# Performance work log

Hardware: AMD Instinct MI355X
Metric: run time of the kernel (lower is better)

The kernel has to match this reference:

```python
import jax, jax.numpy as jnp
import numpy as np

B, V, F = 128, 256, 64      # batch, vertices, features-per-vertex
NS, NLR, K, NOUT = 4, 64, 40, 128
F_EFF = 2 * F               # cat_means doubles feature dim


def setup_inputs() -> dict:
    key = jax.random.key(0)
    k0, k1, k2 = jax.random.split(key, 3)
    x = jax.random.normal(k0, (B, V, F), dtype=jnp.float32)
    # f_slr: single Linear(F_EFF, NS+NLR) + ReLU (f_slr_depth=1)
    W_slr = jax.random.normal(k1, (F_EFF, NS + NLR), dtype=jnp.float32) / np.sqrt(F_EFF).astype(np.float32)
    b_slr = jnp.zeros((NS + NLR,), dtype=jnp.float32)
    # f_out: single Linear(F_EFF + 2*NLR, NOUT) + ReLU (f_out_depth=1, 2 agg methods)
    fin = F_EFF + 2 * NLR
    W_out = jax.random.normal(k2, (fin, NOUT), dtype=jnp.float32) / np.sqrt(fin).astype(np.float32)
    b_out = jnp.zeros((NOUT,), dtype=jnp.float32)
    return {"x": x, "W_slr": W_slr, "b_slr": b_slr, "W_out": W_out, "b_out": b_out}


def reference(x, W_slr, b_slr, W_out, b_out):
    # cat_means: append per-event feature means (broadcast over vertices)
    x = jnp.concatenate([x, jnp.broadcast_to(x.mean(axis=1, keepdims=True), x.shape)], axis=-1)  # (B,V,2F)
    slr = jax.nn.relu(x @ W_slr + b_slr)                    # (B,V,NS+NLR)
    s, lr = slr[..., :NS], slr[..., NS:]
    # pairwise squared distances in latent space (potential only needs d^2, so
    # we skip the sqrt: exp(-10*d^2) == exp(-10*d2), and kNN order is identical)
    diff = s[:, :, None, :] - s[:, None, :, :]              # (B,V,V,NS)
    d2 = jnp.sum(diff * diff, axis=-1)                      # (B,V,V)
    _, idx = jax.lax.top_k(-d2, K)                          # (B,V,K) k smallest (incl. self)
    d2k = jnp.take_along_axis(d2, idx, axis=2)              # (B,V,K)
    lr_nb = jax.vmap(lambda l, i: l[i])(lr, idx)            # (B,V,K,NLR)
    v = jnp.exp(-10.0 * d2k)                                # potential exp(-10 d^2)
    ft = lr_nb * v[..., None]                               # (B,V,K,NLR)
    fp = jnp.concatenate([x, ft.mean(axis=2), ft.max(axis=2)], axis=-1)  # (B,V,2F+2NLR)
    return jax.nn.relu(fp @ W_out + b_out)                  # (B,V,NOUT)
```

## Files before the change

kernel.cpp:

```cpp
#include <hip/hip_runtime.h>

constexpr int Bn = 128, Vn = 256, Fn = 64;
constexpr int NSLR = 68, NSn = 4, NLRn = 64;
constexpr int Kn = 40, NOUTn = 128;
constexpr int ROWS = Bn * Vn;
constexpr int KB2 = 192;

typedef __attribute__((ext_vector_type(8))) short short8;
typedef __attribute__((ext_vector_type(4))) float f32x4;

__device__ __forceinline__ int mbcnt64(unsigned long long m) {
  return __builtin_amdgcn_mbcnt_hi((unsigned)(m >> 32),
         __builtin_amdgcn_mbcnt_lo((unsigned)(m & 0xFFFFFFFFull), 0));
}
__device__ __forceinline__ unsigned short rneb(float v) {
  unsigned u = __float_as_uint(v);
  unsigned r = u + 0x7FFFu + ((u >> 16) & 1u);
  return (unsigned short)(r >> 16);
}
__device__ __forceinline__ float bf2f(unsigned short h) {
  return __uint_as_float(((unsigned)h) << 16);
}
#define GL_LDS(gp, lp) __builtin_amdgcn_global_load_lds( \
    (const __attribute__((address_space(1))) void*)(gp), \
    (__attribute__((address_space(3))) void*)(lp), 16, 0, 0)

__global__ __launch_bounds__(256) void kprep_w(const float* __restrict__ W_slr,
                                               const float* __restrict__ W_out,
                                               short* __restrict__ wt1h, short* __restrict__ wt1l,
                                               short* __restrict__ wt2) {
  const int col = blockIdx.x;
  const int t = threadIdx.x;
  if (t < 64) {
    float val = (col < NSLR) ? W_slr[t * NSLR + col] : 0.f;
    unsigned short h = rneb(val);
    wt1h[col * 64 + t] = (short)h;
    wt1l[col * 64 + t] = (short)rneb(val - bf2f(h));
  } else {
    int k = t - 64;
    int row = (k < 64) ? k : 64 + k;
    wt2[col * KB2 + k] = (short)rneb(W_out[row * NOUTn + col]);
  }
}

__global__ __launch_bounds__(256) void kprep_x(const float* __restrict__ x,
                                               short* __restrict__ xhi, short* __restrict__ xlo,
                                               float* __restrict__ xmean) {
  const int b = blockIdx.x, t = threadIdx.x;
  const int f4 = t & 15, vg = t >> 4;
  const float4* xb = (const float4*)(x + (size_t)b * 16384);
  float4 sum = make_float4(0.f, 0.f, 0.f, 0.f);
  for (int i = 0; i < 16; ++i) {
    int v = vg * 16 + i;
    float4 val = xb[v * 16 + f4];
    sum.x += val.x; sum.y += val.y; sum.z += val.z; sum.w += val.w;
    unsigned short h0 = rneb(val.x), h1 = rneb(val.y), h2 = rneb(val.z), h3 = rneb(val.w);
    short4 hi = {(short)h0, (short)h1, (short)h2, (short)h3};
    short4 lo = {(short)rneb(val.x - bf2f(h0)), (short)rneb(val.y - bf2f(h1)),
                 (short)rneb(val.z - bf2f(h2)), (short)rneb(val.w - bf2f(h3))};
    size_t o = (size_t)b * 4096 + v * 16 + f4;
    ((short4*)xhi)[o] = hi;
    ((short4*)xlo)[o] = lo;
  }
  __shared__ float4 ps[16][16];
  ps[vg][f4] = sum;
  __syncthreads();
  if (t < 16) {
    float4 m = ps[0][t];
    for (int g = 1; g < 16; ++g) {
      float4 v = ps[g][t];
      m.x += v.x; m.y += v.y; m.z += v.z; m.w += v.w;
    }
    m.x *= (1.f / 256.f); m.y *= (1.f / 256.f); m.z *= (1.f / 256.f); m.w *= (1.f / 256.f);
    ((float4*)xmean)[b * 16 + t] = m;
  }
}

__global__ __launch_bounds__(256) void kbias(const float* __restrict__ xmean,
                                             const float* __restrict__ W_slr,
                                             const float* __restrict__ b_slr,
                                             const float* __restrict__ W_out,
                                             const float* __restrict__ b_out,
                                             float* __restrict__ bias1,
                                             float* __restrict__ bias2) {
  const int b = blockIdx.x, t = threadIdx.x;
  __shared__ float xm[64];
  if (t < 64) xm[t] = xmean[b * 64 + t];
  __syncthreads();
  if (t < 128) {
    float acc = b_out[t];
    for (int f = 0; f < 64; ++f) acc = fmaf(xm[f], W_out[(64 + f) * NOUTn + t], acc);
    bias2[b * 128 + t] = acc;
  } else {
    int c = t - 128;
    float acc = 0.f;
    if (c < NSLR) {
      acc = b_slr[c];
      for (int f = 0; f < 64; ++f) acc = fmaf(xm[f], W_slr[(64 + f) * NSLR + c], acc);
    }
    bias1[b * 128 + c] = acc;
  }
}

__global__ __launch_bounds__(256) void kgemm1(
    const short* __restrict__ xhi, const short* __restrict__ xlo,
    const short* __restrict__ wt1h, const short* __restrict__ wt1l,
    const float* __restrict__ bias1,
    float* __restrict__ s_ws, float* __restrict__ lr_ws) {
  __shared__ __align__(16) short Ah[4096], Al[4096], Bh[8192], Bl[8192];
  const int t = threadIdx.x, l = t & 63, w = t >> 6;
  const int wr = w >> 1, wc = w & 1;
  const int rowBase = blockIdx.x * 64;
  const int b = rowBase >> 8;
  const int lr8 = l >> 3, ul = (l & 7) ^ lr8;

#pragma unroll
  for (int rep = 0; rep < 2; ++rep) {
    const int seg = w + rep * 4;
    size_t o = (size_t)(rowBase + seg * 8 + lr8) * 64 + ul * 8;
    GL_LDS(xhi + o, &Ah[seg * 512]);
    GL_LDS(xlo + o, &Al[seg * 512]);
  }
#pragma unroll
  for (int rep = 0; rep < 4; ++rep) {
    const int seg = w + rep * 4;
    size_t o = (size_t)(seg * 8 + lr8) * 64 + ul * 8;
    GL_LDS(wt1h + o, &Bh[seg * 512]);
    GL_LDS(wt1l + o, &Bl[seg * 512]);
  }
  __syncthreads();

  f32x4 acc[2][4];
#pragma unroll
  for (int mf = 0; mf < 2; ++mf)
#pragma unroll
    for (int nf = 0; nf < 4; ++nf) acc[mf][nf] = (f32x4)(0.f);

#pragma unroll
  for (int ks = 0; ks < 2; ++ks) {
    short8 ah[2], al[2], bh[4], bl[4];
#pragma unroll
    for (int mf = 0; mf < 2; ++mf) {
      int row = wr * 32 + mf * 16 + (l & 15);
      int pu = (ks * 4 + (l >> 4)) ^ (row & 7);
      ah[mf] = *(const short8*)&Ah[row * 64 + pu * 8];
      al[mf] = *(const short8*)&Al[row * 64 + pu * 8];
    }
#pragma unroll
    for (int nf = 0; nf < 4; ++nf) {
      int col = wc * 64 + nf * 16 + (l & 15);
      int pu = (ks * 4 + (l >> 4)) ^ (col & 7);
      bh[nf] = *(const short8*)&Bh[col * 64 + pu * 8];
      bl[nf] = *(const short8*)&Bl[col * 64 + pu * 8];
    }
#pragma unroll
    for (int mf = 0; mf < 2; ++mf)
#pragma unroll
      for (int nf = 0; nf < 4; ++nf) {
        acc[mf][nf] = __builtin_amdgcn_mfma_f32_16x16x32_bf16(ah[mf], bh[nf], acc[mf][nf], 0, 0, 0);
        acc[mf][nf] = __builtin_amdgcn_mfma_f32_16x16x32_bf16(ah[mf], bl[nf], acc[mf][nf], 0, 0, 0);
        acc[mf][nf] = __builtin_amdgcn_mfma_f32_16x16x32_bf16(al[mf], bh[nf], acc[mf][nf], 0, 0, 0);
      }
  }
#pragma unroll
  for (int mf = 0; mf < 2; ++mf)
#pragma unroll
    for (int nf = 0; nf < 4; ++nf) {
      const int col = wc * 64 + nf * 16 + (l & 15);
      if (col < NSLR) {
        const float bia = bias1[b * 128 + col];
#pragma unroll
        for (int r = 0; r < 4; ++r) {
          int row = rowBase + wr * 32 + mf * 16 + (l >> 4) * 4 + r;
          float vv = acc[mf][nf][r] + bia;
          vv = vv > 0.f ? vv : 0.f;
          if (col < NSn) s_ws[b * 1024 + col * 256 + (row & 255)] = vv;
          else           lr_ws[(size_t)row * NLRn + (col - NSn)] = vv;
        }
      }
    }
}

__global__ __launch_bounds__(256) void kgemm2(
    const short* __restrict__ xhi, const short* __restrict__ fm,
    const short* __restrict__ fx, const short* __restrict__ wt2,
    const float* __restrict__ bias2, float* __restrict__ outp) {
  __shared__ __align__(16) short As[4096], Bs[8192];
  const int t = threadIdx.x, l = t & 63, w = t >> 6;
  const int wr = w >> 1, wc = w & 1;
  const int rowBase = blockIdx.x * 64;
  const int b = rowBase >> 8;
  const int lr8 = l >> 3, ul = (l & 7) ^ lr8;

  f32x4 acc[2][4];
#pragma unroll
  for (int mf = 0; mf < 2; ++mf)
#pragma unroll
    for (int nf = 0; nf < 4; ++nf) acc[mf][nf] = (f32x4)(0.f);

#pragma unroll
  for (int kc = 0; kc < 3; ++kc) {
    __syncthreads();
    const short* asrc = (kc == 0) ? xhi : (kc == 1) ? fm : fx;
#pragma unroll
    for (int rep = 0; rep < 2; ++rep) {
      const int seg = w + rep * 4;
      size_t o = (size_t)(rowBase + seg * 8 + lr8) * 64 + ul * 8;
      GL_LDS(asrc + o, &As[seg * 512]);
    }
#pragma unroll
    for (int rep = 0; rep < 4; ++rep) {
      const int seg = w + rep * 4;
      size_t o = (size_t)(seg * 8 + lr8) * KB2 + kc * 64 + ul * 8;
      GL_LDS(wt2 + o, &Bs[seg * 512]);
    }
    __syncthreads();
#pragma unroll
    for (int ks = 0; ks < 2; ++ks) {
      short8 a[2], bb[4];
#pragma unroll
      for (int mf = 0; mf < 2; ++mf) {
        int row = wr * 32 + mf * 16 + (l & 15);
        int pu = (ks * 4 + (l >> 4)) ^ (row & 7);
        a[mf] = *(const short8*)&As[row * 64 + pu * 8];
      }
#pragma unroll
      for (int nf = 0; nf < 4; ++nf) {
        int col = wc * 64 + nf * 16 + (l & 15);
        int pu = (ks * 4 + (l >> 4)) ^ (col & 7);
        bb[nf] = *(const short8*)&Bs[col * 64 + pu * 8];
      }
#pragma unroll
      for (int mf = 0; mf < 2; ++mf)
#pragma unroll
        for (int nf = 0; nf < 4; ++nf)
          acc[mf][nf] = __builtin_amdgcn_mfma_f32_16x16x32_bf16(a[mf], bb[nf], acc[mf][nf], 0, 0, 0);
    }
  }
#pragma unroll
  for (int mf = 0; mf < 2; ++mf)
#pragma unroll
    for (int nf = 0; nf < 4; ++nf) {
      const int col = wc * 64 + nf * 16 + (l & 15);
      const float bia = bias2[b * 128 + col];
#pragma unroll
      for (int r = 0; r < 4; ++r) {
        int row = rowBase + wr * 32 + mf * 16 + (l >> 4) * 4 + r;
        float vv = acc[mf][nf][r] + bia;
        outp[(size_t)row * NOUTn + col] = vv > 0.f ? vv : 0.f;
      }
    }
}

__global__ __launch_bounds__(256) void kselect(const float* __restrict__ s_ws,
                                               const float* __restrict__ lr_ws,
                                               short* __restrict__ fm,
                                               short* __restrict__ fx) {
  __shared__ float sT[4][256];
  __shared__ unsigned int lst[4][Kn];
  const int id = blockIdx.x;
  const int xcd = id & 7;
  const int rrx = id >> 3;
  const int b = xcd + 8 * (rrx & 15);
  const int seg = rrx >> 4;
  const int t = threadIdx.x, lane = t & 63, w = t >> 6;

  {
    const float* sb = s_ws + b * 1024;
    sT[0][t] = sb[t]; sT[1][t] = sb[256 + t];
    sT[2][t] = sb[512 + t]; sT[3][t] = sb[768 + t];
  }
  __syncthreads();

  const float C = -14.4269504088896340736f;
  const float* lrbase = lr_ws + (size_t)b * (256 * NLRn) + lane;

  for (int it = 0; it < 4; ++it) {
    const int i = seg * 16 + w * 4 + it;
    const float si0 = sT[0][i], si1 = sT[1][i];
    const float si2 = sT[2][i], si3 = sT[3][i];
    unsigned int kb[4];
    float vv[4];
#pragma unroll
    for (int q = 0; q < 4; ++q) {
      int j = q * 64 + lane;
      float d0 = sT[0][j] - si0;
      float d1 = sT[1][j] - si1;
      float d2_ = sT[2][j] - si2;
      float d3 = sT[3][j] - si3;
      float dd = ((d0 * d0 + d1 * d1) + d2_ * d2_) + d3 * d3;
      kb[q] = __float_as_uint(dd);
      vv[q] = exp2f(C * dd);
    }
    unsigned int T = 0;
    for (int bit = 30; bit >= 0; --bit) {
      unsigned int cand = T | (1u << bit);
      int cnt = __popcll(__ballot(kb[0] < cand)) + __popcll(__ballot(kb[1] < cand)) +
                __popcll(__ballot(kb[2] < cand)) + __popcll(__ballot(kb[3] < cand));
      if (cnt < Kn) T = cand;
    }
    int nlt = __popcll(__ballot(kb[0] < T)) + __popcll(__ballot(kb[1] < T)) +
              __popcll(__ballot(kb[2] < T)) + __popcll(__ballot(kb[3] < T));
    int rem = Kn - nlt;
    int base = 0, ecum = 0;
#pragma unroll
    for (int q = 0; q < 4; ++q) {
      bool lt = kb[q] < T;
      bool eq = kb[q] == T;
      unsigned long long meq = __ballot(eq);
      int eqrank = ecum + mbcnt64(meq);
      bool sel = lt || (eq && (eqrank < rem));
      unsigned long long msel = __ballot(sel);
      int pos = base + mbcnt64(msel);
      if (sel)
        lst[w][pos] = (__float_as_uint(vv[q]) & 0xFFFFFF00u) | (unsigned)(q * 64 + lane);
      base += __popcll(msel);
      ecum += __popcll(meq);
    }
    float accm = 0.f, accx = 0.f;
#pragma unroll 8
    for (int tt = 0; tt < Kn; ++tt) {
      unsigned int p = lst[w][tt];
      int j = p & 0xFF;
      float v = __uint_as_float(p & 0xFFFFFF00u);
      float tv = v * lrbase[j * NLRn];
      accm += tv;
      accx = fmaxf(accx, tv);
    }
    size_t ro = ((size_t)(b * 256 + i)) * 64 + lane;
    fm[ro] = (short)rneb(accm * (1.f / 40.f));
    fx[ro] = (short)rneb(accx);
  }
}

extern "C" void kernel_launch(void* const* d_in, const int* in_sizes, int n_in,
                              void* d_out, int out_size, void* d_ws, size_t ws_size,
                              hipStream_t stream) {
  const float* x = (const float*)d_in[0];
  const float* W_slr = (const float*)d_in[1];
  const float* b_slr = (const float*)d_in[2];
  const float* W_out = (const float*)d_in[3];
  const float* b_out = (const float*)d_in[4];
  float* out = (float*)d_out;

  char* p = (char*)d_ws;
  auto take = [&](size_t bytes) { char* c = p; p += (bytes + 255) & ~(size_t)255; return c; };
  short* xhi = (short*)take((size_t)ROWS * 64 * 2);
  short* xlo = (short*)take((size_t)ROWS * 64 * 2);
  float* xmean = (float*)take(Bn * 64 * 4);
  short* wt1h = (short*)take(128 * 64 * 2);
  short* wt1l = (short*)take(128 * 64 * 2);
  short* wt2 = (short*)take(128 * KB2 * 2);
  float* bias1 = (float*)take(Bn * 128 * 4);
  float* bias2 = (float*)take(Bn * 128 * 4);
  float* s_ws = (float*)take(Bn * 1024 * 4);
  float* lr_ws = (float*)take((size_t)ROWS * 64 * 4);
  short* fm = (short*)take((size_t)ROWS * 64 * 2);
  short* fx = (short*)take((size_t)ROWS * 64 * 2);

  kprep_w<<<128, 256, 0, stream>>>(W_slr, W_out, wt1h, wt1l, wt2);
  kprep_x<<<Bn, 256, 0, stream>>>(x, xhi, xlo, xmean);
  kbias<<<Bn, 256, 0, stream>>>(xmean, W_slr, b_slr, W_out, b_out, bias1, bias2);
  kgemm1<<<ROWS / 64, 256, 0, stream>>>(xhi, xlo, wt1h, wt1l, bias1, s_ws, lr_ws);
  kselect<<<Bn * 16, 256, 0, stream>>>(s_ws, lr_ws, fm, fx);
  kgemm2<<<ROWS / 64, 256, 0, stream>>>(xhi, fm, fx, wt2, bias2, out);
}
```

Baseline: 133.6 us.

## Fuse prep kernels, limit split-bf16 to s columns, batch kNN radix selects per wave

Merges the weight-prep, x-prep and bias kernels into one launch, with the per-batch mean kept in LDS instead of a global buffer. In gemm1 the hi/lo split-bf16 correction MFMAs now run only on the first column tile, which holds the 4 s columns, so the lr outputs become plain bf16. kselect now handles its four rows per wave together: it interleaves the bit-by-bit threshold searches to expose ILP and gathers the neighbour features for all four rows in one loop. This trims launch overhead and MFMA work, at the cost of lower precision on lr and higher register pressure in kselect.

```diff
diff --git a/kernel.cpp b/kernel.cpp
--- a/kernel.cpp
+++ b/kernel.cpp
@@ -25,28 +25,29 @@
     (const __attribute__((address_space(1))) void*)(gp), \
     (__attribute__((address_space(3))) void*)(lp), 16, 0, 0)
 
-__global__ __launch_bounds__(256) void kprep_w(const float* __restrict__ W_slr,
-                                               const float* __restrict__ W_out,
-                                               short* __restrict__ wt1h, short* __restrict__ wt1l,
-                                               short* __restrict__ wt2) {
-  const int col = blockIdx.x;
-  const int t = threadIdx.x;
-  if (t < 64) {
-    float val = (col < NSLR) ? W_slr[t * NSLR + col] : 0.f;
-    unsigned short h = rneb(val);
-    wt1h[col * 64 + t] = (short)h;
-    wt1l[col * 64 + t] = (short)rneb(val - bf2f(h));
-  } else {
-    int k = t - 64;
-    int row = (k < 64) ? k : 64 + k;
-    wt2[col * KB2 + k] = (short)rneb(W_out[row * NOUTn + col]);
-  }
-}
-
-__global__ __launch_bounds__(256) void kprep_x(const float* __restrict__ x,
-                                               short* __restrict__ xhi, short* __restrict__ xlo,
-                                               float* __restrict__ xmean) {
-  const int b = blockIdx.x, t = threadIdx.x;
+__global__ __launch_bounds__(256) void kprep(
+    const float* __restrict__ x,
+    const float* __restrict__ W_slr, const float* __restrict__ b_slr,
+    const float* __restrict__ W_out, const float* __restrict__ b_out,
+    short* __restrict__ xhi, short* __restrict__ xlo,
+    short* __restrict__ wt1h, short* __restrict__ wt1l, short* __restrict__ wt2,
+    float* __restrict__ bias1, float* __restrict__ bias2) {
+  const int blk = blockIdx.x, t = threadIdx.x;
+  if (blk >= Bn) {
+    const int col = blk - Bn;
+    if (t < 64) {
+      float val = (col < NSLR) ? W_slr[t * NSLR + col] : 0.f;
+      unsigned short h = rneb(val);
+      wt1h[col * 64 + t] = (short)h;
+      wt1l[col * 64 + t] = (short)rneb(val - bf2f(h));
+    } else {
+      int k = t - 64;
+      int row = (k < 64) ? k : 64 + k;
+      wt2[col * KB2 + k] = (short)rneb(W_out[row * NOUTn + col]);
+    }
+    return;
+  }
+  const int b = blk;
   const int f4 = t & 15, vg = t >> 4;
   const float4* xb = (const float4*)(x + (size_t)b * 16384);
   float4 sum = make_float4(0.f, 0.f, 0.f, 0.f);
@@ -63,6 +64,7 @@
     ((short4*)xlo)[o] = lo;
   }
   __shared__ float4 ps[16][16];
+  __shared__ float xms[64];
   ps[vg][f4] = sum;
   __syncthreads();
   if (t < 16) {
@@ -72,33 +74,20 @@
       m.x += v.x; m.y += v.y; m.z += v.z; m.w += v.w;
     }
     m.x *= (1.f / 256.f); m.y *= (1.f / 256.f); m.z *= (1.f / 256.f); m.w *= (1.f / 256.f);
-    ((float4*)xmean)[b * 16 + t] = m;
-  }
-}
-
-__global__ __launch_bounds__(256) void kbias(const float* __restrict__ xmean,
-                                             const float* __restrict__ W_slr,
-                                             const float* __restrict__ b_slr,
-                                             const float* __restrict__ W_out,
-                                             const float* __restrict__ b_out,
-                                             float* __restrict__ bias1,
-                                             float* __restrict__ bias2) {
-  const int b = blockIdx.x, t = threadIdx.x;
-  __shared__ float xm[64];
-  if (t < 64) xm[t] = xmean[b * 64 + t];
+    ((float4*)xms)[t] = m;
+  }
   __syncthreads();
   if (t < 128) {
     float acc = b_out[t];
-    for (int f = 0; f < 64; ++f) acc = fmaf(xm[f], W_out[(64 + f) * NOUTn + t], acc);
+    for (int f = 0; f < 64; ++f) acc = fmaf(xms[f], W_out[(64 + f) * NOUTn + t], acc);
     bias2[b * 128 + t] = acc;
   } else {
     int c = t - 128;
-    float acc = 0.f;
     if (c < NSLR) {
-      acc = b_slr[c];
-      for (int f = 0; f < 64; ++f) acc = fmaf(xm[f], W_slr[(64 + f) * NSLR + c], acc);
-    }
-    bias1[b * 128 + c] = acc;
+      float acc = b_slr[c];
+      for (int f = 0; f < 64; ++f) acc = fmaf(xms[f], W_slr[(64 + f) * NSLR + c], acc);
+      bias1[b * 128 + c] = acc;
+    }
   }
 }
 
@@ -107,7 +96,7 @@
     const short* __restrict__ wt1h, const short* __restrict__ wt1l,
     const float* __restrict__ bias1,
     float* __restrict__ s_ws, float* __restrict__ lr_ws) {
-  __shared__ __align__(16) short Ah[4096], Al[4096], Bh[8192], Bl[8192];
+  __shared__ __align__(16) short Ah[4096], Al[4096], Bh[8192], Bl[1024];
   const int t = threadIdx.x, l = t & 63, w = t >> 6;
   const int wr = w >> 1, wc = w & 1;
   const int rowBase = blockIdx.x * 64;
@@ -126,7 +115,10 @@
     const int seg = w + rep * 4;
     size_t o = (size_t)(seg * 8 + lr8) * 64 + ul * 8;
     GL_LDS(wt1h + o, &Bh[seg * 512]);
-    GL_LDS(wt1l + o, &Bl[seg * 512]);
+  }
+  if (w < 2) {
+    size_t o = (size_t)(w * 8 + lr8) * 64 + ul * 8;
+    GL_LDS(wt1l + o, &Bl[w * 512]);
   }
   __syncthreads();
 
@@ -138,29 +130,37 @@
 
 #pragma unroll
   for (int ks = 0; ks < 2; ++ks) {
-    short8 ah[2], al[2], bh[4], bl[4];
+    short8 ah[2], bh[4];
 #pragma unroll
     for (int mf = 0; mf < 2; ++mf) {
       int row = wr * 32 + mf * 16 + (l & 15);
       int pu = (ks * 4 + (l >> 4)) ^ (row & 7);
       ah[mf] = *(const short8*)&Ah[row * 64 + pu * 8];
-      al[mf] = *(const short8*)&Al[row * 64 + pu * 8];
     }
 #pragma unroll
     for (int nf = 0; nf < 4; ++nf) {
       int col = wc * 64 + nf * 16 + (l & 15);
       int pu = (ks * 4 + (l >> 4)) ^ (col & 7);
       bh[nf] = *(const short8*)&Bh[col * 64 + pu * 8];
-      bl[nf] = *(const short8*)&Bl[col * 64 + pu * 8];
     }
 #pragma unroll
     for (int mf = 0; mf < 2; ++mf)
 #pragma unroll
-      for (int nf = 0; nf < 4; ++nf) {
+      for (int nf = 0; nf < 4; ++nf)
         acc[mf][nf] = __builtin_amdgcn_mfma_f32_16x16x32_bf16(ah[mf], bh[nf], acc[mf][nf], 0, 0, 0);
-        acc[mf][nf] = __builtin_amdgcn_mfma_f32_16x16x32_bf16(ah[mf], bl[nf], acc[mf][nf], 0, 0, 0);
-        acc[mf][nf] = __builtin_amdgcn_mfma_f32_16x16x32_bf16(al[mf], bh[nf], acc[mf][nf], 0, 0, 0);
-      }
+    if (wc == 0) {
+      int col0 = l & 15;
+      int puc = (ks * 4 + (l >> 4)) ^ (col0 & 7);
+      short8 bl0 = *(const short8*)&Bl[col0 * 64 + puc * 8];
+#pragma unroll
+      for (int mf = 0; mf < 2; ++mf) {
+        int row = wr * 32 + mf * 16 + (l & 15);
+        int pu = (ks * 4 + (l >> 4)) ^ (row & 7);
+        short8 al = *(const short8*)&Al[row * 64 + pu * 8];
+        acc[mf][0] = __builtin_amdgcn_mfma_f32_16x16x32_bf16(ah[mf], bl0, acc[mf][0], 0, 0, 0);
+        acc[mf][0] = __builtin_amdgcn_mfma_f32_16x16x32_bf16(al, bh[0], acc[mf][0], 0, 0, 0);
+      }
+    }
   }
 #pragma unroll
   for (int mf = 0; mf < 2; ++mf)
@@ -252,12 +252,17 @@
     }
 }
 
+__device__ __forceinline__ int cntlt(const unsigned* kbr, unsigned c) {
+  return __popcll(__ballot(kbr[0] < c)) + __popcll(__ballot(kbr[1] < c)) +
+         __popcll(__ballot(kbr[2] < c)) + __popcll(__ballot(kbr[3] < c));
+}
+
 __global__ __launch_bounds__(256) void kselect(const float* __restrict__ s_ws,
                                                const float* __restrict__ lr_ws,
                                                short* __restrict__ fm,
                                                short* __restrict__ fx) {
   __shared__ float sT[4][256];
-  __shared__ unsigned int lst[4][Kn];
+  __shared__ unsigned int lst[4][4][Kn];
   const int id = blockIdx.x;
   const int xcd = id & 7;
   const int rrx = id >> 3;
@@ -272,64 +277,86 @@
   }
   __syncthreads();
 
+  float sj[4][4];
+#pragma unroll
+  for (int q = 0; q < 4; ++q)
+#pragma unroll
+    for (int c = 0; c < 4; ++c) sj[q][c] = sT[c][q * 64 + lane];
+
   const float C = -14.4269504088896340736f;
-  const float* lrbase = lr_ws + (size_t)b * (256 * NLRn) + lane;
-
-  for (int it = 0; it < 4; ++it) {
-    const int i = seg * 16 + w * 4 + it;
-    const float si0 = sT[0][i], si1 = sT[1][i];
-    const float si2 = sT[2][i], si3 = sT[3][i];
-    unsigned int kb[4];
-    float vv[4];
+  unsigned kb[4][4];
+  float vv[4][4];
+#pragma unroll
+  for (int r = 0; r < 4; ++r) {
+    const int i = seg * 16 + w * 4 + r;
+    const float si0 = sT[0][i], si1 = sT[1][i], si2 = sT[2][i], si3 = sT[3][i];
 #pragma unroll
     for (int q = 0; q < 4; ++q) {
-      int j = q * 64 + lane;
-      float d0 = sT[0][j] - si0;
-      float d1 = sT[1][j] - si1;
-      float d2_ = sT[2][j] - si2;
-      float d3 = sT[3][j] - si3;
+      float d0 = sj[q][0] - si0;
+      float d1 = sj[q][1] - si1;
+      float d2_ = sj[q][2] - si2;
+      float d3 = sj[q][3] - si3;
       float dd = ((d0 * d0 + d1 * d1) + d2_ * d2_) + d3 * d3;
-      kb[q] = __float_as_uint(dd);
-      vv[q] = exp2f(C * dd);
-    }
-    unsigned int T = 0;
-    for (int bit = 30; bit >= 0; --bit) {
-      unsigned int cand = T | (1u << bit);
-      int cnt = __popcll(__ballot(kb[0] < cand)) + __popcll(__ballot(kb[1] < cand)) +
-                __popcll(__ballot(kb[2] < cand)) + __popcll(__ballot(kb[3] < cand));
-      if (cnt < Kn) T = cand;
-    }
-    int nlt = __popcll(__ballot(kb[0] < T)) + __popcll(__ballot(kb[1] < T)) +
-              __popcll(__ballot(kb[2] < T)) + __popcll(__ballot(kb[3] < T));
+      kb[r][q] = __float_as_uint(dd);
+      vv[r][q] = exp2f(C * dd);
+    }
+  }
+  unsigned T[4] = {0u, 0u, 0u, 0u};
+#pragma unroll 1
+  for (int bit = 30; bit >= 0; --bit) {
+    const unsigned m = 1u << bit;
+    unsigned c0 = T[0] | m, c1 = T[1] | m, c2 = T[2] | m, c3 = T[3] | m;
+    int n0 = cntlt(kb[0], c0);
+    int n1 = cntlt(kb[1], c1);
+    int n2 = cntlt(kb[2], c2);
+    int n3 = cntlt(kb[3], c3);
+    T[0] = (n0 < Kn) ? c0 : T[0];
+    T[1] = (n1 < Kn) ? c1 : T[1];
+    T[2] = (n2 < Kn) ? c2 : T[2];
+    T[3] = (n3 < Kn) ? c3 : T[3];
+  }
+#pragma unroll
+  for (int r = 0; r < 4; ++r) {
+    const unsigned Tr = T[r];
+    int nlt = cntlt(kb[r], Tr);
     int rem = Kn - nlt;
     int base = 0, ecum = 0;
 #pragma unroll
     for (int q = 0; q < 4; ++q) {
-      bool lt = kb[q] < T;
-      bool eq = kb[q] == T;
+      bool lt = kb[r][q] < Tr;
+      bool eq = kb[r][q] == Tr;
       unsigned long long meq = __ballot(eq);
       int eqrank = ecum + mbcnt64(meq);
       bool sel = lt || (eq && (eqrank < rem));
       unsigned long long msel = __ballot(sel);
       int pos = base + mbcnt64(msel);
       if (sel)
-        lst[w][pos] = (__float_as_uint(vv[q]) & 0xFFFFFF00u) | (unsigned)(q * 64 + lane);
+        lst[w][r][pos] = (__float_as_uint(vv[r][q]) & 0xFFFFFF00u) | (unsigned)(q * 64 + lane);
       base += __popcll(msel);
       ecum += __popcll(meq);
     }
-    float accm = 0.f, accx = 0.f;
-#pragma unroll 8
-    for (int tt = 0; tt < Kn; ++tt) {
-      unsigned int p = lst[w][tt];
+  }
+  float accm[4] = {0.f, 0.f, 0.f, 0.f};
+  float accx[4] = {0.f, 0.f, 0.f, 0.f};
+  const float* lrb = lr_ws + (size_t)b * (256 * NLRn) + lane;
+#pragma unroll 4
+  for (int tt = 0; tt < Kn; ++tt) {
+#pragma unroll
+    for (int r = 0; r < 4; ++r) {
+      unsigned p = lst[w][r][tt];
       int j = p & 0xFF;
       float v = __uint_as_float(p & 0xFFFFFF00u);
-      float tv = v * lrbase[j * NLRn];
-      accm += tv;
-      accx = fmaxf(accx, tv);
-    }
+      float tv = v * lrb[j * NLRn];
+      accm[r] += tv;
+      accx[r] = fmaxf(accx[r], tv);
+    }
+  }
+#pragma unroll
+  for (int r = 0; r < 4; ++r) {
+    const int i = seg * 16 + w * 4 + r;
     size_t ro = ((size_t)(b * 256 + i)) * 64 + lane;
-    fm[ro] = (short)rneb(accm * (1.f / 40.f));
-    fx[ro] = (short)rneb(accx);
+    fm[ro] = (short)rneb(accm[r] * (1.f / 40.f));
+    fx[ro] = (short)rneb(accx[r]);
   }
 }
 
@@ -347,7 +374,6 @@
   auto take = [&](size_t bytes) { char* c = p; p += (bytes + 255) & ~(size_t)255; return c; };
   short* xhi = (short*)take((size_t)ROWS * 64 * 2);
   short* xlo = (short*)take((size_t)ROWS * 64 * 2);
-  float* xmean = (float*)take(Bn * 64 * 4);
   short* wt1h = (short*)take(128 * 64 * 2);
   short* wt1l = (short*)take(128 * 64 * 2);
   short* wt2 = (short*)take(128 * KB2 * 2);
@@ -358,9 +384,8 @@
   short* fm = (short*)take((size_t)ROWS * 64 * 2);
   short* fx = (short*)take((size_t)ROWS * 64 * 2);
 
-  kprep_w<<<128, 256, 0, stream>>>(W_slr, W_out, wt1h, wt1l, wt2);
-  kprep_x<<<Bn, 256, 0, stream>>>(x, xhi, xlo, xmean);
-  kbias<<<Bn, 256, 0, stream>>>(xmean, W_slr, b_slr, W_out, b_out, bias1, bias2);
+  kprep<<<256, 256, 0, stream>>>(x, W_slr, b_slr, W_out, b_out,
+                                 xhi, xlo, wt1h, wt1l, wt2, bias1, bias2);
   kgemm1<<<ROWS / 64, 256, 0, stream>>>(xhi, xlo, wt1h, wt1l, bias1, s_ws, lr_ws);
   kselect<<<Bn * 16, 256, 0, stream>>>(s_ws, lr_ws, fm, fx);
   kgemm2<<<ROWS / 64, 256, 0, stream>>>(xhi, fm, fx, wt2, bias2, out);
```

After: 130.6 us. 2.2% less time.
